# Kernel optimization log

Measured on AMD Instinct MI355X. Metric: run time of the kernel, lower is better.

## Reference

```python
import jax, jax.numpy as jnp
import numpy as np

B, NW, D, K = 16384, 32, 64, 512  # batch, n_windows, embedding_dim, codebook_size


def setup_inputs() -> dict:
    key = jax.random.key(0)
    k1, k2 = jax.random.split(key)
    ze = jax.random.normal(k1, (B, NW * D), dtype=jnp.float32)
    codebook = jax.random.normal(k2, (K, D), dtype=jnp.float32)
    return {"ze": ze, "codebook": codebook}


def reference(ze, codebook):
    # window-based VQ: split last dim into NW windows of size D, quantize each
    zew = ze.reshape(B, NW, D)
    # squared distances: ||ze||^2 + ||e||^2 - 2 ze.e^T  -> [B, NW, K]
    sq_norm = (
        jnp.sum(zew * zew, axis=-1, keepdims=True)
        + jnp.sum(codebook * codebook, axis=-1)
        - 2.0 * jnp.einsum("bwd,kd->bwk", zew, codebook)
    )
    indices = jnp.argmin(sq_norm, axis=-1)  # [B, NW]
    zq = codebook[indices].reshape(ze.shape)  # gather + concat over windows

    vq_e_loss = jnp.mean((zq - jax.lax.stop_gradient(ze)) ** 2)
    vq_commit_loss = jnp.mean((jax.lax.stop_gradient(zq) - ze) ** 2)

    # entropy term: counts of each code usage divided by 10 (as in original)
    counts = jnp.bincount(indices.reshape(-1), length=K)
    probs = counts.astype(jnp.float32) / 10.0
    entropy = jnp.sum(probs * jnp.log(probs + 1e-10))
    return indices, zq, vq_e_loss, vq_commit_loss, entropy
```

## Files before the change

### kernel.cpp

```cpp
#include <hip/hip_runtime.h>
#include <math.h>

#define DIM 64
#define KCB 512
#define NWIN 524288
#define ZQN (NWIN * DIM)
#define WPB 256
#define NBLK (NWIN / WPB)

typedef __attribute__((ext_vector_type(8))) short bf16x8;
typedef __attribute__((ext_vector_type(4))) float f32x4;

__device__ __forceinline__ unsigned bfbits(float f) { return __float_as_uint(f) >> 16; }

__device__ __forceinline__ int4 pack8(float4 a, float4 b) {
    int4 r;
    r.x = (int)(bfbits(a.x) | (__float_as_uint(a.y) & 0xffff0000u));
    r.y = (int)(bfbits(a.z) | (__float_as_uint(a.w) & 0xffff0000u));
    r.z = (int)(bfbits(b.x) | (__float_as_uint(b.y) & 0xffff0000u));
    r.w = (int)(bfbits(b.z) | (__float_as_uint(b.w) & 0xffff0000u));
    return r;
}

__global__ __launch_bounds__(256, 4) void vq_fused_kernel(
    const float* __restrict__ ze, const float* __restrict__ cb,
    float* __restrict__ out_idx, float* __restrict__ zq,
    int* __restrict__ counts, float* __restrict__ lossAcc)
{
    __shared__ int4  bfr[2048];
    __shared__ float norm_s[KCB];
    __shared__ int   idx_s[WPB];
    __shared__ int   hist_s[KCB];
    __shared__ float lpart[4];

    const int t    = threadIdx.x;
    const int lane = t & 63;
    const int wv   = t >> 6;
    const int q    = lane >> 4;
    const int l15  = lane & 15;
    const long blk = blockIdx.x;

    hist_s[t] = 0; hist_s[t + 256] = 0;

    {
        const float4* c4 = (const float4*)cb;
        for (int rr = t; rr < KCB; rr += 256) {
            float s = 0.f;
#pragma unroll
            for (int i = 0; i < 16; ++i) {
                float4 v = c4[rr * 16 + i];
                s += v.x * v.x + v.y * v.y + v.z * v.z + v.w * v.w;
            }
            norm_s[rr] = s;
        }
    }

    bf16x8 afrag[4][2];
    float  znorm[4];
    {
        const float4* z4 = (const float4*)(ze + blk * WPB * DIM);
#pragma unroll
        for (int tt = 0; tt < 4; ++tt) {
            float part = 0.f;
            int m = wv * 64 + tt * 16 + l15;
#pragma unroll
            for (int h = 0; h < 2; ++h) {
                int off = m * 16 + h * 8 + q * 2;
                float4 a0 = z4[off], a1 = z4[off + 1];
                part += a0.x*a0.x + a0.y*a0.y + a0.z*a0.z + a0.w*a0.w
                      + a1.x*a1.x + a1.y*a1.y + a1.z*a1.z + a1.w*a1.w;
                int4 p = pack8(a0, a1);
                afrag[tt][h] = __builtin_bit_cast(bf16x8, p);
            }
            part += __shfl_xor(part, 16, 64);
            part += __shfl_xor(part, 32, 64);
            znorm[tt] = part;
        }
    }

    float best[4][4];
#pragma unroll
    for (int tt = 0; tt < 4; ++tt)
#pragma unroll
        for (int r = 0; r < 4; ++r) best[tt][r] = __uint_as_float(0x7e000000u);

    for (int half = 0; half < 2; ++half) {
        __syncthreads();
#pragma unroll
        for (int i = 0; i < 8; ++i) {
            int f = i * 256 + t;
            int L = f & 63, rest = f >> 6, h = rest & 1, c = rest >> 1;
            int n = half * 256 + c * 16 + (L & 15);
            int k = h * 32 + (L >> 4) * 8;
            const float4* s4 = (const float4*)(cb + n * DIM + k);
            bfr[(c * 2 + h) * 64 + L] = pack8(s4[0], s4[1]);
        }
        __syncthreads();

        for (int c = 0; c < 16; ++c) {
            bf16x8 b0 = __builtin_bit_cast(bf16x8, bfr[(c * 2 + 0) * 64 + lane]);
            bf16x8 b1 = __builtin_bit_cast(bf16x8, bfr[(c * 2 + 1) * 64 + lane]);
            int   n   = half * 256 + c * 16 + l15;
            float nrm = norm_s[n];
#pragma unroll
            for (int tt = 0; tt < 4; ++tt) {
                f32x4 acc = {0.f, 0.f, 0.f, 0.f};
                acc = __builtin_amdgcn_mfma_f32_16x16x32_bf16(afrag[tt][0], b0, acc, 0, 0, 0);
                acc = __builtin_amdgcn_mfma_f32_16x16x32_bf16(afrag[tt][1], b1, acc, 0, 0, 0);
#pragma unroll
                for (int r = 0; r < 4; ++r) {
                    float sc = fmaf(nrm, 0.5f, -acc[r]);
                    unsigned bb = (__float_as_uint(sc) & ~511u) | (unsigned)n;
                    best[tt][r] = fminf(best[tt][r], __uint_as_float(bb));
                }
            }
        }
    }

#pragma unroll
    for (int tt = 0; tt < 4; ++tt)
#pragma unroll
        for (int r = 0; r < 4; ++r) {
            float v = best[tt][r];
            v = fminf(v, __shfl_xor(v, 1, 64));
            v = fminf(v, __shfl_xor(v, 2, 64));
            v = fminf(v, __shfl_xor(v, 4, 64));
            v = fminf(v, __shfl_xor(v, 8, 64));
            best[tt][r] = v;
        }

    float lsum = 0.f;
    int  r_act = l15 - q * 4;
    bool act   = (r_act >= 0) && (r_act < 4);
#pragma unroll
    for (int tt = 0; tt < 4; ++tt) {
        if (act) {
            unsigned bb = __float_as_uint(best[tt][r_act]);
            int   n  = (int)(bb & 511u);
            float sc = __uint_as_float(bb & ~511u);
            float d2 = fmaf(2.f, sc, znorm[tt]);
            int w_loc = wv * 64 + tt * 16 + l15;
            idx_s[w_loc] = n;
            out_idx[blk * WPB + w_loc] = (float)n;
            lsum += d2;
        }
    }
#pragma unroll
    for (int off = 32; off; off >>= 1) lsum += __shfl_down(lsum, off, 64);
    if (lane == 0) lpart[wv] = lsum;
    __syncthreads();

    atomicAdd(&hist_s[idx_s[t]], 1);
    if (t == 0) atomicAdd(lossAcc, lpart[0] + lpart[1] + lpart[2] + lpart[3]);

    {
        const float4* c4  = (const float4*)cb;
        float4*       zq4 = (float4*)zq;
        const long base = blk * WPB * 16;
#pragma unroll
        for (int it = 0; it < 16; ++it) {
            int w_loc = it * 16 + (t >> 4);
            int n = idx_s[w_loc];
            zq4[base + (long)w_loc * 16 + (t & 15)] = c4[n * 16 + (t & 15)];
        }
    }
    __syncthreads();
    int h0 = hist_s[t], h1 = hist_s[t + 256];
    if (h0) atomicAdd(&counts[t], h0);
    if (h1) atomicAdd(&counts[t + 256], h1);
}

__global__ __launch_bounds__(512) void vq_finalize_kernel(
    const int* __restrict__ counts, const float* __restrict__ lossAcc,
    float* __restrict__ outs)
{
    __shared__ float partial[8];
    const int t = threadIdx.x;

    float p = (float)counts[t] * 0.1f;
    float term = p * logf(p + 1e-10f);
#pragma unroll
    for (int off = 32; off; off >>= 1) term += __shfl_down(term, off, 64);
    if ((t & 63) == 0) partial[t >> 6] = term;
    __syncthreads();
    if (t == 0) {
        float e = 0.f;
#pragma unroll
        for (int i = 0; i < 8; ++i) e += partial[i];
        float loss = lossAcc[0] / (float)ZQN;
        outs[0] = loss;
        outs[1] = loss;
        outs[2] = e;
    }
}

extern "C" void kernel_launch(void* const* d_in, const int* in_sizes, int n_in,
                              void* d_out, int out_size, void* d_ws, size_t ws_size,
                              hipStream_t stream) {
    const float* ze = (const float*)d_in[0];
    const float* cb = (const float*)d_in[1];
    float* out = (float*)d_out;

    float* out_idx = out;
    float* out_zq  = out + NWIN;
    float* out_scl = out + NWIN + (long)ZQN;

    int*   counts  = (int*)d_ws;
    float* lossAcc = (float*)((char*)d_ws + KCB * sizeof(int));
    hipMemsetAsync(d_ws, 0, KCB * sizeof(int) + sizeof(float), stream);

    vq_fused_kernel<<<NBLK, 256, 0, stream>>>(ze, cb, out_idx, out_zq, counts, lossAcc);
    vq_finalize_kernel<<<1, KCB, 0, stream>>>(counts, lossAcc, out_scl);
}
```

Before: 291.6 us.

## Stage full bf16 codebook once per block and loop over four window tiles

Each block now converts the whole 512-entry codebook to bf16 in LDS once, then processes four 256-window tiles in turn. The next tile's ze values are prefetched into registers while the current tile computes. zq is gathered from the bf16 LDS copy instead of re-reading fp32 codebook rows from global memory. This amortises codebook staging and removes the per-half barriers, at the cost of doubled LDS and half the occupancy bound. zq values are now bf16-truncated rather than exact codebook entries, which risks failing output tolerance.

After: 285.2 us. 2.2% less time.

```diff
diff --git a/kernel.cpp b/kernel.cpp
--- a/kernel.cpp
+++ b/kernel.cpp
@@ -5,8 +5,9 @@
 #define KCB 512
 #define NWIN 524288
 #define ZQN (NWIN * DIM)
-#define WPB 256
-#define NBLK (NWIN / WPB)
+#define WPT 256
+#define TPB 4
+#define NBLK (NWIN / (WPT * TPB))
 
 typedef __attribute__((ext_vector_type(8))) short bf16x8;
 typedef __attribute__((ext_vector_type(4))) float f32x4;
@@ -22,14 +23,14 @@
     return r;
 }
 
-__global__ __launch_bounds__(256, 4) void vq_fused_kernel(
+__global__ __launch_bounds__(256, 2) void vq_fused_kernel(
     const float* __restrict__ ze, const float* __restrict__ cb,
     float* __restrict__ out_idx, float* __restrict__ zq,
     int* __restrict__ counts, float* __restrict__ lossAcc)
 {
-    __shared__ int4  bfr[2048];
+    __shared__ int4  bfr[4096];
     __shared__ float norm_s[KCB];
-    __shared__ int   idx_s[WPB];
+    __shared__ int   idx_s[WPT];
     __shared__ int   hist_s[KCB];
     __shared__ float lpart[4];
 
@@ -55,52 +56,80 @@
         }
     }
 
-    bf16x8 afrag[4][2];
-    float  znorm[4];
+#pragma unroll
+    for (int i = 0; i < 16; ++i) {
+        int f = i * 256 + t;
+        int L = f & 63, rest = f >> 6, h = rest & 1, c = rest >> 1;
+        int n = c * 16 + (L & 15);
+        int k = h * 32 + (L >> 4) * 8;
+        const float4* s4 = (const float4*)(cb + n * DIM + k);
+        bfr[(c * 2 + h) * 64 + L] = pack8(s4[0], s4[1]);
+    }
+    __syncthreads();
+
+    const float4* z4b = (const float4*)ze;
+    float4*       zq4 = (float4*)zq;
+    float lsum = 0.f;
+
+    float4 abuf[16];
     {
-        const float4* z4 = (const float4*)(ze + blk * WPB * DIM);
+        const float4* z4 = z4b + blk * TPB * WPT * 16;
+#pragma unroll
+        for (int tt = 0; tt < 4; ++tt)
+#pragma unroll
+            for (int h = 0; h < 2; ++h)
+#pragma unroll
+                for (int i = 0; i < 2; ++i) {
+                    int m = wv * 64 + tt * 16 + l15;
+                    abuf[tt * 4 + h * 2 + i] = z4[m * 16 + h * 8 + q * 2 + i];
+                }
+    }
+
+#pragma unroll
+    for (int tl = 0; tl < TPB; ++tl) {
+        const long g = blk * TPB + tl;
+
+        float4 pre[16];
+        if (tl < TPB - 1) {
+            const float4* z4 = z4b + (g + 1) * WPT * 16;
+#pragma unroll
+            for (int tt = 0; tt < 4; ++tt)
+#pragma unroll
+                for (int h = 0; h < 2; ++h)
+#pragma unroll
+                    for (int i = 0; i < 2; ++i) {
+                        int m = wv * 64 + tt * 16 + l15;
+                        pre[tt * 4 + h * 2 + i] = z4[m * 16 + h * 8 + q * 2 + i];
+                    }
+        }
+
+        bf16x8 afrag[4][2];
+        float  znorm[4];
 #pragma unroll
         for (int tt = 0; tt < 4; ++tt) {
             float part = 0.f;
-            int m = wv * 64 + tt * 16 + l15;
 #pragma unroll
             for (int h = 0; h < 2; ++h) {
-                int off = m * 16 + h * 8 + q * 2;
-                float4 a0 = z4[off], a1 = z4[off + 1];
+                float4 a0 = abuf[tt * 4 + h * 2], a1 = abuf[tt * 4 + h * 2 + 1];
                 part += a0.x*a0.x + a0.y*a0.y + a0.z*a0.z + a0.w*a0.w
                       + a1.x*a1.x + a1.y*a1.y + a1.z*a1.z + a1.w*a1.w;
-                int4 p = pack8(a0, a1);
-                afrag[tt][h] = __builtin_bit_cast(bf16x8, p);
+                afrag[tt][h] = __builtin_bit_cast(bf16x8, pack8(a0, a1));
             }
             part += __shfl_xor(part, 16, 64);
             part += __shfl_xor(part, 32, 64);
             znorm[tt] = part;
         }
-    }
-
-    float best[4][4];
-#pragma unroll
-    for (int tt = 0; tt < 4; ++tt)
-#pragma unroll
-        for (int r = 0; r < 4; ++r) best[tt][r] = __uint_as_float(0x7e000000u);
-
-    for (int half = 0; half < 2; ++half) {
-        __syncthreads();
-#pragma unroll
-        for (int i = 0; i < 8; ++i) {
-            int f = i * 256 + t;
-            int L = f & 63, rest = f >> 6, h = rest & 1, c = rest >> 1;
-            int n = half * 256 + c * 16 + (L & 15);
-            int k = h * 32 + (L >> 4) * 8;
-            const float4* s4 = (const float4*)(cb + n * DIM + k);
-            bfr[(c * 2 + h) * 64 + L] = pack8(s4[0], s4[1]);
-        }
-        __syncthreads();
-
-        for (int c = 0; c < 16; ++c) {
+
+        float best[4][4];
+#pragma unroll
+        for (int tt = 0; tt < 4; ++tt)
+#pragma unroll
+            for (int r = 0; r < 4; ++r) best[tt][r] = __uint_as_float(0x7e000000u);
+
+        for (int c = 0; c < 32; ++c) {
             bf16x8 b0 = __builtin_bit_cast(bf16x8, bfr[(c * 2 + 0) * 64 + lane]);
             bf16x8 b1 = __builtin_bit_cast(bf16x8, bfr[(c * 2 + 1) * 64 + lane]);
-            int   n   = half * 256 + c * 16 + l15;
+            int   n   = c * 16 + l15;
             float nrm = norm_s[n];
 #pragma unroll
             for (int tt = 0; tt < 4; ++tt) {
@@ -115,56 +144,73 @@
                 }
             }
         }
-    }
-
-#pragma unroll
-    for (int tt = 0; tt < 4; ++tt)
-#pragma unroll
-        for (int r = 0; r < 4; ++r) {
-            float v = best[tt][r];
-            v = fminf(v, __shfl_xor(v, 1, 64));
-            v = fminf(v, __shfl_xor(v, 2, 64));
-            v = fminf(v, __shfl_xor(v, 4, 64));
-            v = fminf(v, __shfl_xor(v, 8, 64));
-            best[tt][r] = v;
-        }
-
-    float lsum = 0.f;
-    int  r_act = l15 - q * 4;
-    bool act   = (r_act >= 0) && (r_act < 4);
-#pragma unroll
-    for (int tt = 0; tt < 4; ++tt) {
-        if (act) {
-            unsigned bb = __float_as_uint(best[tt][r_act]);
-            int   n  = (int)(bb & 511u);
-            float sc = __uint_as_float(bb & ~511u);
-            float d2 = fmaf(2.f, sc, znorm[tt]);
-            int w_loc = wv * 64 + tt * 16 + l15;
-            idx_s[w_loc] = n;
-            out_idx[blk * WPB + w_loc] = (float)n;
-            lsum += d2;
-        }
-    }
+
+#pragma unroll
+        for (int tt = 0; tt < 4; ++tt)
+#pragma unroll
+            for (int r = 0; r < 4; ++r) {
+                float v = best[tt][r];
+                v = fminf(v, __shfl_xor(v, 1, 64));
+                v = fminf(v, __shfl_xor(v, 2, 64));
+                v = fminf(v, __shfl_xor(v, 4, 64));
+                v = fminf(v, __shfl_xor(v, 8, 64));
+                best[tt][r] = v;
+            }
+
+        {
+            int  r_act = l15 - q * 4;
+            bool act   = (r_act >= 0) && (r_act < 4);
+#pragma unroll
+            for (int tt = 0; tt < 4; ++tt) {
+                if (act) {
+                    unsigned bb = __float_as_uint(best[tt][r_act]);
+                    int   n  = (int)(bb & 511u);
+                    float sc = __uint_as_float(bb & ~511u);
+                    lsum += fmaf(2.f, sc, znorm[tt]);
+                    idx_s[wv * 64 + tt * 16 + l15] = n;
+                }
+            }
+        }
+        __syncthreads();
+
+        out_idx[g * WPT + t] = (float)idx_s[t];
+        atomicAdd(&hist_s[idx_s[t]], 1);
+
+        {
+            const long zb = g * WPT * 16;
+#pragma unroll
+            for (int it = 0; it < 16; ++it) {
+                int w_loc = it * 16 + (t >> 4);
+                int j  = t & 15;
+                int n  = idx_s[w_loc];
+                int c  = n >> 4, ln = n & 15;
+                int h  = j >> 3;
+                int q2 = (j >> 1) & 3;
+                int4 v = bfr[(c * 2 + h) * 64 + q2 * 16 + ln];
+                int a  = (j & 1) ? v.z : v.x;
+                int b  = (j & 1) ? v.w : v.y;
+                float4 o;
+                o.x = __uint_as_float((unsigned)a << 16);
+                o.y = __uint_as_float((unsigned)a & 0xffff0000u);
+                o.z = __uint_as_float((unsigned)b << 16);
+                o.w = __uint_as_float((unsigned)b & 0xffff0000u);
+                zq4[zb + (long)w_loc * 16 + j] = o;
+            }
+        }
+        __syncthreads();
+
+        if (tl < TPB - 1) {
+#pragma unroll
+            for (int i = 0; i < 16; ++i) abuf[i] = pre[i];
+        }
+    }
+
 #pragma unroll
     for (int off = 32; off; off >>= 1) lsum += __shfl_down(lsum, off, 64);
     if (lane == 0) lpart[wv] = lsum;
     __syncthreads();
-
-    atomicAdd(&hist_s[idx_s[t]], 1);
     if (t == 0) atomicAdd(lossAcc, lpart[0] + lpart[1] + lpart[2] + lpart[3]);
 
-    {
-        const float4* c4  = (const float4*)cb;
-        float4*       zq4 = (float4*)zq;
-        const long base = blk * WPB * 16;
-#pragma unroll
-        for (int it = 0; it < 16; ++it) {
-            int w_loc = it * 16 + (t >> 4);
-            int n = idx_s[w_loc];
-            zq4[base + (long)w_loc * 16 + (t & 15)] = c4[n * 16 + (t & 15)];
-        }
-    }
-    __syncthreads();
     int h0 = hist_s[t], h1 = hist_s[t + 256];
     if (h0) atomicAdd(&counts[t], h0);
     if (h1) atomicAdd(&counts[t + 256], h1);
```
